# Kernel tuning notes

Hardware: AMD Instinct MI355X
Metric: run time of the kernel (lower is better)

The kernel has to match this reference:

```python
import jax, jax.numpy as jnp
import numpy as np

K = 4096          # infeatures
N = 12288         # outfeatures
M = 4096          # tokens (batch*seq)
GROUPSIZE = 128
G = K // GROUPSIZE  # 32 groups
PACK = 8          # 8 int4 nibbles per int32


def _unpack_int4(q):
    """Unpack int32 [R, C] -> int32 [R, C*8]; nibble j of word c maps to column c*8+j."""
    shifts = jnp.arange(0, 32, 4, dtype=jnp.int32)          # [8]
    nib = (q[:, :, None] >> shifts[None, None, :]) & 0xF    # [R, C, 8]
    return nib.reshape(q.shape[0], -1)


def setup_inputs() -> dict:
    key = jax.random.key(0)
    k1, k2, k3, k4, k5 = jax.random.split(key, 5)
    x = jax.random.normal(k1, (M, K), dtype=jnp.float32)
    qweight = jax.random.randint(k2, (K, N // PACK), 0, 2147483647, dtype=jnp.int32)
    qzeros = jax.random.randint(k3, (G, N // PACK), 0, 2147483647, dtype=jnp.int32)
    scales = jax.random.uniform(k4, (G, N), dtype=jnp.float32, minval=0.001, maxval=0.01)
    bias = jax.random.normal(k5, (N,), dtype=jnp.float32)
    return {"x": x, "qweight": qweight, "qzeros": qzeros, "scales": scales,
            "bias": bias, "groupsize": GROUPSIZE}


def reference(x, qweight, qzeros, scales, bias, groupsize):
    # Dequantize: w[k, n] = (q4[k, n] - z4[k//gs, n]) * scales[k//gs, n]
    w_int = _unpack_int4(qweight)                 # [K, N] int32, values 0..15
    z_int = _unpack_int4(qzeros)                  # [G, N] int32 (+1 already folded in)
    z_full = jnp.repeat(z_int, groupsize, axis=0)      # [K, N]
    s_full = jnp.repeat(scales, groupsize, axis=0)     # [K, N]
    weight = (w_int - z_full).astype(x.dtype) * s_full  # [K, N]
    out = x @ weight + bias                        # [M, N]
    return out
```

## Files before the change

### kernel.cpp

```cpp
#include <hip/hip_runtime.h>

#define M_DIM 4096
#define N_DIM 12288
#define K_DIM 4096
#define NP    1536
#define GS    128

typedef unsigned short ushort_t;
typedef _Float16 half8 __attribute__((ext_vector_type(8)));
typedef unsigned short us8 __attribute__((ext_vector_type(8)));
typedef float f32x16 __attribute__((ext_vector_type(16)));
typedef float f32x4 __attribute__((ext_vector_type(4)));

__device__ __forceinline__ unsigned short f2h(float f) {
  _Float16 h = (_Float16)f;
  return __builtin_bit_cast(unsigned short, h);
}

#define GLDS16(G, L) __builtin_amdgcn_global_load_lds(                      \
    (const __attribute__((address_space(1))) void*)(G),                     \
    (__attribute__((address_space(3))) void*)(L), 16, 0, 0)

#define DQ_BLOCKS (96 * 64)
#define CVT_BLOCKS (M_DIM * K_DIM / 16 / 256)

__global__ __launch_bounds__(256) void prep_kernel(
    const int* __restrict__ qw, const int* __restrict__ qz,
    const float* __restrict__ sc, ushort_t* __restrict__ wt,
    const float* __restrict__ x, ushort_t* __restrict__ xb) {
  __shared__ int ldsQ[64 * 16];
  __shared__ int ldsZ[16];
  const int tid = threadIdx.x;
  if (blockIdx.x >= DQ_BLOCKS) {
    size_t cid = (size_t)(blockIdx.x - DQ_BLOCKS) * 256 + tid;
    const float4* p = (const float4*)(x + cid * 16);
    float4 a = p[0], b = p[1], c = p[2], d = p[3];
    us8 o0, o1;
    o0[0] = f2h(a.x); o0[1] = f2h(a.y); o0[2] = f2h(a.z); o0[3] = f2h(a.w);
    o0[4] = f2h(b.x); o0[5] = f2h(b.y); o0[6] = f2h(b.z); o0[7] = f2h(b.w);
    o1[0] = f2h(c.x); o1[1] = f2h(c.y); o1[2] = f2h(c.z); o1[3] = f2h(c.w);
    o1[4] = f2h(d.x); o1[5] = f2h(d.y); o1[6] = f2h(d.z); o1[7] = f2h(d.w);
    *(us8*)(xb + cid * 16)     = o0;
    *(us8*)(xb + cid * 16 + 8) = o1;
    return;
  }
  const int bx = blockIdx.x % 96;
  const int by = blockIdx.x / 96;
  const int k0 = by * 64;
  const int n0 = bx * 128;
  const int w0 = n0 >> 3;
  const int g  = k0 >> 7;
  {
    int row = tid >> 2, qc = tid & 3;
    int4 v = *(const int4*)(qw + (size_t)(k0 + row) * NP + w0 + qc * 4);
    ldsQ[row * 16 + ((qc * 4 + 0) ^ (row & 15))] = v.x;
    ldsQ[row * 16 + ((qc * 4 + 1) ^ (row & 15))] = v.y;
    ldsQ[row * 16 + ((qc * 4 + 2) ^ (row & 15))] = v.z;
    ldsQ[row * 16 + ((qc * 4 + 3) ^ (row & 15))] = v.w;
  }
  if (tid < 16) ldsZ[tid] = qz[g * NP + w0 + tid];
  __syncthreads();
  const int nl  = tid >> 1;
  const int kh  = tid & 1;
  const int col = nl >> 3;
  const int j4  = (nl & 7) * 4;
  const int z   = (ldsZ[col] >> j4) & 0xF;
  const float s = sc[(size_t)g * N_DIM + n0 + nl];
  ushort_t* dst = wt + (size_t)(n0 + nl) * K_DIM + k0 + kh * 32;
#pragma unroll
  for (int c = 0; c < 4; ++c) {
    us8 o;
#pragma unroll
    for (int ii = 0; ii < 8; ++ii) {
      int row = kh * 32 + c * 8 + ii;
      int q = (ldsQ[row * 16 + (col ^ (row & 15))] >> j4) & 0xF;
      o[ii] = f2h((float)(q - z) * s);
    }
    *(us8*)(dst + c * 8) = o;
  }
}


__device__ __forceinline__ void stage_unit(
    int u, const ushort_t* __restrict__ Ag, const ushort_t* __restrict__ Bg,
    int m0, int n0, int tid, ushort_t* lds) {
  const int t   = u >> 1;
  const int ks  = u & 1;
  const int b   = t & 1;
  const int kbu = t * 64 + ks * 32;
  const int r   = tid >> 1;
  const int hp  = (tid & 1) ^ ((tid >> 3) & 1);
  const size_t ka = (size_t)kbu + hp * 8;
  ushort_t* dA = lds + b * 32768 + (2 * ks) * 4096 + tid * 8;
  ushort_t* dB = dA + 16384;
  const ushort_t* sA = Ag + (size_t)(m0 + r) * K_DIM + ka;
  const ushort_t* sB = Bg + (size_t)(n0 + r) * K_DIM + ka;
  GLDS16(sA,      dA);
  GLDS16(sA + 16, dA + 4096);
  GLDS16(sB,      dB);
  GLDS16(sB + 16, dB + 4096);
}

template <int N>
__device__ __forceinline__ void wait_lgkm() {
  if constexpr (N == 0)      asm volatile("s_waitcnt lgkmcnt(0)" ::: "memory");
  else if constexpr (N == 1) asm volatile("s_waitcnt lgkmcnt(1)" ::: "memory");
  else if constexpr (N == 2) asm volatile("s_waitcnt lgkmcnt(2)" ::: "memory");
  else if constexpr (N == 3) asm volatile("s_waitcnt lgkmcnt(3)" ::: "memory");
  else if constexpr (N == 4) asm volatile("s_waitcnt lgkmcnt(4)" ::: "memory");
  else if constexpr (N == 5) asm volatile("s_waitcnt lgkmcnt(5)" ::: "memory");
  else if constexpr (N == 6) asm volatile("s_waitcnt lgkmcnt(6)" ::: "memory");
  else if constexpr (N == 7) asm volatile("s_waitcnt lgkmcnt(7)" ::: "memory");
  __builtin_amdgcn_sched_barrier(0);
}

#define SB() __builtin_amdgcn_sched_barrier(0)

template <int VN, bool STG>
__device__ __forceinline__ void gemm_phase(
    int p, const ushort_t* __restrict__ Ag, const ushort_t* __restrict__ Bg,
    int m0, int n0, int tid, ushort_t* lds, f32x4 (&acc)[8][4]) {
  const int lane = tid & 63;
  const int wid  = tid >> 6;
  const int wm   = wid & 1;
  const int wn   = wid >> 1;
  const int ks   = p & 1;
  const int b    = (p >> 1) & 1;
  const int c  = lane >> 4;
  const int rl = lane & 15;
  const int sg = (c & 1) ^ ((rl >> 2) & 1);
  const ushort_t* base = lds + b * 32768 + (2 * ks + (c >> 1)) * 4096 + sg * 8;
  const ushort_t* pa = base + (wm * 128 + rl) * 16;
  const ushort_t* pb = base + 16384 + (wn * 64 + rl) * 16;
  half8 af[8], bf[4];
  af[0] = *(const half8*)(pa);
  bf[0] = *(const half8*)(pb);
  bf[1] = *(const half8*)(pb + 256);
  bf[2] = *(const half8*)(pb + 512);
  bf[3] = *(const half8*)(pb + 768);
  SB();
  af[1] = *(const half8*)(pa + 256);  SB();
  af[2] = *(const half8*)(pa + 512);  SB();
  af[3] = *(const half8*)(pa + 768);  SB();
  af[4] = *(const half8*)(pa + 1024); SB();
  af[5] = *(const half8*)(pa + 1280); SB();
  af[6] = *(const half8*)(pa + 1536); SB();
  af[7] = *(const half8*)(pa + 1792); SB();
  if constexpr (STG) stage_unit(p + 3, Ag, Bg, m0, n0, tid, lds);
  __builtin_amdgcn_s_setprio(1);
#define MFMA_ROW(i, W)                                                       \
  wait_lgkm<W>();                                                            \
  acc[i][0] = __builtin_amdgcn_mfma_f32_16x16x32_f16(af[i], bf[0], acc[i][0], 0, 0, 0); \
  acc[i][1] = __builtin_amdgcn_mfma_f32_16x16x32_f16(af[i], bf[1], acc[i][1], 0, 0, 0); \
  acc[i][2] = __builtin_amdgcn_mfma_f32_16x16x32_f16(af[i], bf[2], acc[i][2], 0, 0, 0); \
  acc[i][3] = __builtin_amdgcn_mfma_f32_16x16x32_f16(af[i], bf[3], acc[i][3], 0, 0, 0)
  MFMA_ROW(0, 7);
  MFMA_ROW(1, 6);
  MFMA_ROW(2, 5);
  MFMA_ROW(3, 4);
  MFMA_ROW(4, 3);
  MFMA_ROW(5, 2);
  MFMA_ROW(6, 1);
  MFMA_ROW(7, 0);
#undef MFMA_ROW
  __builtin_amdgcn_s_setprio(0);
  if constexpr (VN == 8)      asm volatile("s_waitcnt vmcnt(8)" ::: "memory");
  else if constexpr (VN == 4) asm volatile("s_waitcnt vmcnt(4)" ::: "memory");
  else if constexpr (VN == 0) asm volatile("s_waitcnt vmcnt(0)" ::: "memory");
  if constexpr (VN >= 0) {
    __builtin_amdgcn_s_barrier();
    asm volatile("" ::: "memory");
  }
}

__global__ __launch_bounds__(512, 2) void gemm256_kernel(
    const ushort_t* __restrict__ Xb, const ushort_t* __restrict__ Wt,
    const float* __restrict__ bias, float* __restrict__ out) {
  __shared__ __align__(16) ushort_t lds[65536];
  const int tid = threadIdx.x;
  const int m0  = blockIdx.x * 256;
  const int n0  = blockIdx.y * 256;
  f32x4 acc[8][4] = {};

  stage_unit(0, Xb, Wt, m0, n0, tid, lds);
  stage_unit(1, Xb, Wt, m0, n0, tid, lds);
  stage_unit(2, Xb, Wt, m0, n0, tid, lds);
  asm volatile("s_waitcnt vmcnt(8)" ::: "memory");
  __builtin_amdgcn_s_barrier();
  asm volatile("" ::: "memory");

#pragma unroll 4
  for (int p = 0; p < 125; ++p)
    gemm_phase<8, true>(p, Xb, Wt, m0, n0, tid, lds, acc);
  gemm_phase<4,  false>(125, Xb, Wt, m0, n0, tid, lds, acc);
  gemm_phase<0,  false>(126, Xb, Wt, m0, n0, tid, lds, acc);
  gemm_phase<-1, false>(127, Xb, Wt, m0, n0, tid, lds, acc);

  const int lane = tid & 63;
  const int wm   = (tid >> 6) & 1;
  const int wn   = tid >> 7;
#pragma unroll
  for (int jj = 0; jj < 4; ++jj) {
    int n = n0 + wn * 64 + jj * 16 + (lane & 15);
    float bv = bias[n];
#pragma unroll
    for (int i = 0; i < 8; ++i) {
      int mb = (int)(m0 + wm * 128 + i * 16 + ((lane >> 4) << 2));
#pragma unroll
      for (int r = 0; r < 4; ++r)
        __builtin_nontemporal_store(acc[i][jj][r] + bv,
                                    out + (size_t)(mb + r) * N_DIM + n);
    }
  }
}

template <int APRE, int BPRE>
__global__ __launch_bounds__(256) void gemm_kernel(
    const ushort_t* __restrict__ Xb, const float* __restrict__ Xf,
    const ushort_t* __restrict__ Wt,
    const int* __restrict__ qw, const int* __restrict__ qz,
    const float* __restrict__ sc,
    const float* __restrict__ bias, float* __restrict__ out) {
  __shared__ __align__(16) ushort_t lsA[128 * 64];
  __shared__ __align__(16) ushort_t lsB[128 * 64];
  const int tid  = threadIdx.x;
  const int lane = tid & 63;
  const int wid  = tid >> 6;
  const int wm   = wid & 1;
  const int wn   = wid >> 1;
  const int m0   = blockIdx.x * 128;
  const int n0   = blockIdx.y * 128;

  f32x16 acc[2][2] = {};

  for (int kt = 0; kt < K_DIM / 64; ++kt) {
    const int kb = kt * 64;
    if constexpr (APRE) {
#pragma unroll
      for (int i = 0; i < 4; ++i) {
        int cid = i * 256 + tid;
        int r = cid >> 3, scol = cid & 7;
        int c = scol ^ (r & 7);
        GLDS16(Xb + (size_t)(m0 + r) * K_DIM + kb + c * 8, lsA + cid * 8);
      }
    } else {
#pragma unroll
      for (int i = 0; i < 4; ++i) {
        int cid = i * 256 + tid;
        int r = cid >> 3, scol = cid & 7;
        int c = scol ^ (r & 7);
        const float* src = Xf + (size_t)(m0 + r) * K_DIM + kb + c * 8;
        float4 a = *(const float4*)src;
        float4 b = *(const float4*)(src + 4);
        us8 o;
        o[0] = f2h(a.x); o[1] = f2h(a.y); o[2] = f2h(a.z); o[3] = f2h(a.w);
        o[4] = f2h(b.x); o[5] = f2h(b.y); o[6] = f2h(b.z); o[7] = f2h(b.w);
        *(us8*)(lsA + cid * 8) = o;
      }
    }
    if constexpr (BPRE) {
#pragma unroll
      for (int i = 0; i < 4; ++i) {
        int cid = i * 256 + tid;
        int r = cid >> 3, scol = cid & 7;
        int c = scol ^ (r & 7);
        GLDS16(Wt + (size_t)(n0 + r) * K_DIM + kb + c * 8, lsB + cid * 8);
      }
    } else {
#pragma unroll
      for (int i = 0; i < 4; ++i) {
        int wi = i * 256 + tid;
        int kl = wi >> 4, cw = wi & 15;
        int k = kb + kl;
        int g = k >> 7;
        int qword = qw[(size_t)k * NP + (n0 >> 3) + cw];
        int zword = qz[g * NP + (n0 >> 3) + cw];
        float4 s0 = *(const float4*)(sc + (size_t)g * N_DIM + n0 + cw * 8);
        float4 s1 = *(const float4*)(sc + (size_t)g * N_DIM + n0 + cw * 8 + 4);
        float sv[8] = {s0.x, s0.y, s0.z, s0.w, s1.x, s1.y, s1.z, s1.w};
#pragma unroll
        for (int j = 0; j < 8; ++j) {
          int nl = cw * 8 + j;
          int q = (qword >> (4 * j)) & 0xF;
          int z = (zword >> (4 * j)) & 0xF;
          lsB[nl * 64 + (((kl >> 3) ^ (nl & 7)) << 3) + (kl & 7)] =
              f2h((float)(q - z) * sv[j]);
        }
      }
    }
    __syncthreads();
#pragma unroll
    for (int ks = 0; ks < 4; ++ks) {
      half8 af[2], bfr[2];
      const int h = lane >> 5;
      const int c = ks * 2 + h;
#pragma unroll
      for (int i = 0; i < 2; ++i) {
        int row = wm * 64 + i * 32 + (lane & 31);
        af[i] = *(const half8*)(lsA + (row * 8 + (c ^ (row & 7))) * 8);
      }
#pragma unroll
      for (int jj = 0; jj < 2; ++jj) {
        int row = wn * 64 + jj * 32 + (lane & 31);
        bfr[jj] = *(const half8*)(lsB + (row * 8 + (c ^ (row & 7))) * 8);
      }
#pragma unroll
      for (int i = 0; i < 2; ++i)
#pragma unroll
        for (int jj = 0; jj < 2; ++jj)
          acc[i][jj] = __builtin_amdgcn_mfma_f32_32x32x16_f16(
              af[i], bfr[jj], acc[i][jj], 0, 0, 0);
    }
    __syncthreads();
  }

#pragma unroll
  for (int jj = 0; jj < 2; ++jj) {
    int n = n0 + wn * 64 + jj * 32 + (lane & 31);
    float bv = bias[n];
#pragma unroll
    for (int i = 0; i < 2; ++i) {
      int mbase = m0 + wm * 64 + i * 32 + ((lane >> 5) << 2);
#pragma unroll
      for (int reg = 0; reg < 16; ++reg) {
        int m = mbase + (reg & 3) + ((reg >> 2) << 3);
        __builtin_nontemporal_store(acc[i][jj][reg] + bv,
                                    out + (size_t)m * N_DIM + n);
      }
    }
  }
}

extern "C" void kernel_launch(void* const* d_in, const int* in_sizes, int n_in,
                              void* d_out, int out_size, void* d_ws, size_t ws_size,
                              hipStream_t stream) {
  const float* x    = (const float*)d_in[0];
  const int*   qw   = (const int*)d_in[1];
  const int*   qz   = (const int*)d_in[2];
  const float* sc   = (const float*)d_in[3];
  const float* bias = (const float*)d_in[4];
  float*       out  = (float*)d_out;

  const size_t WT_BYTES = (size_t)N_DIM * K_DIM * 2;
  const size_t XB_BYTES = (size_t)M_DIM * K_DIM * 2;
  ushort_t* Wt = (ushort_t*)d_ws;
  ushort_t* Xb = (ushort_t*)((char*)d_ws + WT_BYTES);
  const bool hasWt = ws_size >= WT_BYTES;
  const bool hasXb = ws_size >= WT_BYTES + XB_BYTES;

  if (hasXb) {
    prep_kernel<<<DQ_BLOCKS + CVT_BLOCKS, 256, 0, stream>>>(qw, qz, sc, Wt, x, Xb);
    dim3 grid256(M_DIM / 256, N_DIM / 256);
    gemm256_kernel<<<grid256, 512, 0, stream>>>(Xb, Wt, bias, out);
  } else if (hasWt) {
    dim3 grid(M_DIM / 128, N_DIM / 128);
    prep_kernel<<<DQ_BLOCKS, 256, 0, stream>>>(qw, qz, sc, Wt, x, nullptr);
    gemm_kernel<0, 1><<<grid, 256, 0, stream>>>(nullptr, x, Wt, qw, qz, sc, bias, out);
  } else {
    dim3 grid(M_DIM / 128, N_DIM / 128);
    gemm_kernel<0, 0><<<grid, 256, 0, stream>>>(nullptr, x, nullptr, qw, qz, sc, bias, out);
  }
}
```

Measured before the change: 638.9 us.

## Pre-tile fp16 operands into LDS-ready swizzled blocks for contiguous staging

The prep kernel now writes dequantized weights and fp16 activations in a tiled layout. Each 256-row by 32-k slab is stored contiguously with the LDS swizzle baked in. The GEMM staging loads therefore become fully contiguous 16-byte global-to-LDS copies instead of strided row reads. The intent is better global load coalescing and simpler address math in the main loop, in exchange for a more complex prep-side shuffle. The unused intermediate fallback path is also removed.

```diff
diff --git a/kernel.cpp b/kernel.cpp
--- a/kernel.cpp
+++ b/kernel.cpp
@@ -9,6 +9,7 @@
 typedef unsigned short ushort_t;
 typedef _Float16 half8 __attribute__((ext_vector_type(8)));
 typedef unsigned short us8 __attribute__((ext_vector_type(8)));
+typedef unsigned short us16 __attribute__((ext_vector_type(16)));
 typedef float f32x16 __attribute__((ext_vector_type(16)));
 typedef float f32x4 __attribute__((ext_vector_type(4)));
 
@@ -21,84 +22,100 @@
     (const __attribute__((address_space(1))) void*)(G),                     \
     (__attribute__((address_space(3))) void*)(L), 16, 0, 0)
 
-#define DQ_BLOCKS (96 * 64)
-#define CVT_BLOCKS (M_DIM * K_DIM / 16 / 256)
+
+#define DQ_BLOCKS (48 * 128)
+#define CVT_BLOCKS (16 * 128)
 
 __global__ __launch_bounds__(256) void prep_kernel(
     const int* __restrict__ qw, const int* __restrict__ qz,
-    const float* __restrict__ sc, ushort_t* __restrict__ wt,
-    const float* __restrict__ x, ushort_t* __restrict__ xb) {
-  __shared__ int ldsQ[64 * 16];
-  __shared__ int ldsZ[16];
+    const float* __restrict__ sc, ushort_t* __restrict__ wtT,
+    const float* __restrict__ x, ushort_t* __restrict__ xbT) {
+  __shared__ int ldsQ[32 * 32];
+  __shared__ int ldsZ[32];
   const int tid = threadIdx.x;
-  if (blockIdx.x >= DQ_BLOCKS) {
-    size_t cid = (size_t)(blockIdx.x - DQ_BLOCKS) * 256 + tid;
-    const float4* p = (const float4*)(x + cid * 16);
-    float4 a = p[0], b = p[1], c = p[2], d = p[3];
-    us8 o0, o1;
-    o0[0] = f2h(a.x); o0[1] = f2h(a.y); o0[2] = f2h(a.z); o0[3] = f2h(a.w);
-    o0[4] = f2h(b.x); o0[5] = f2h(b.y); o0[6] = f2h(b.z); o0[7] = f2h(b.w);
-    o1[0] = f2h(c.x); o1[1] = f2h(c.y); o1[2] = f2h(c.z); o1[3] = f2h(c.w);
-    o1[4] = f2h(d.x); o1[5] = f2h(d.y); o1[6] = f2h(d.z); o1[7] = f2h(d.w);
-    *(us8*)(xb + cid * 16)     = o0;
-    *(us8*)(xb + cid * 16 + 8) = o1;
+  const int bx  = blockIdx.x;
+  if (bx >= DQ_BLOCKS) {
+    const int idx = bx - DQ_BLOCKS;
+    const int pm = idx >> 7, u = idx & 127;
+    const int r  = tid;
+    const int rb = (r >> 2) & 1;
+    const float* src = x + (size_t)(pm * 256 + r) * K_DIM + u * 32;
+    ushort_t* dst = xbT + (size_t)(pm * 128 + u) * 8192 + r * 16;
+#pragma unroll
+    for (int sl = 0; sl < 2; ++sl) {
+      float4 f0 = *(const float4*)(src + sl * 16);
+      float4 f1 = *(const float4*)(src + sl * 16 + 4);
+      float4 f2 = *(const float4*)(src + sl * 16 + 8);
+      float4 f3 = *(const float4*)(src + sl * 16 + 12);
+      us8 lo, hi;
+      lo[0] = f2h(f0.x); lo[1] = f2h(f0.y); lo[2] = f2h(f0.z); lo[3] = f2h(f0.w);
+      lo[4] = f2h(f1.x); lo[5] = f2h(f1.y); lo[6] = f2h(f1.z); lo[7] = f2h(f1.w);
+      hi[0] = f2h(f2.x); hi[1] = f2h(f2.y); hi[2] = f2h(f2.z); hi[3] = f2h(f2.w);
+      hi[4] = f2h(f3.x); hi[5] = f2h(f3.y); hi[6] = f2h(f3.z); hi[7] = f2h(f3.w);
+      us8 s0 = rb ? hi : lo;
+      us8 s1 = rb ? lo : hi;
+      us16 o = __builtin_shufflevector(s0, s1, 0, 1, 2, 3, 4, 5, 6, 7,
+                                       8, 9, 10, 11, 12, 13, 14, 15);
+      *(us16*)(dst + sl * 4096) = o;
+    }
     return;
   }
-  const int bx = blockIdx.x % 96;
-  const int by = blockIdx.x / 96;
-  const int k0 = by * 64;
-  const int n0 = bx * 128;
-  const int w0 = n0 >> 3;
-  const int g  = k0 >> 7;
+  const int p  = bx >> 7;
+  const int u  = bx & 127;
+  const int w0 = p << 5;
+  const int g  = u >> 2;
+  const int kb = u << 5;
   {
-    int row = tid >> 2, qc = tid & 3;
-    int4 v = *(const int4*)(qw + (size_t)(k0 + row) * NP + w0 + qc * 4);
-    ldsQ[row * 16 + ((qc * 4 + 0) ^ (row & 15))] = v.x;
-    ldsQ[row * 16 + ((qc * 4 + 1) ^ (row & 15))] = v.y;
-    ldsQ[row * 16 + ((qc * 4 + 2) ^ (row & 15))] = v.z;
-    ldsQ[row * 16 + ((qc * 4 + 3) ^ (row & 15))] = v.w;
-  }
-  if (tid < 16) ldsZ[tid] = qz[g * NP + w0 + tid];
+    int row = tid >> 3, wq = tid & 7;
+    int4 v = *(const int4*)(qw + (size_t)(kb + row) * NP + w0 + wq * 4);
+    ldsQ[row * 32 + ((wq * 4 + 0) ^ row)] = v.x;
+    ldsQ[row * 32 + ((wq * 4 + 1) ^ row)] = v.y;
+    ldsQ[row * 32 + ((wq * 4 + 2) ^ row)] = v.z;
+    ldsQ[row * 32 + ((wq * 4 + 3) ^ row)] = v.w;
+  }
+  if (tid < 32) ldsZ[tid] = qz[(size_t)g * NP + w0 + tid];
   __syncthreads();
-  const int nl  = tid >> 1;
-  const int kh  = tid & 1;
-  const int col = nl >> 3;
-  const int j4  = (nl & 7) * 4;
+  const int r   = tid;
+  const int col = r >> 3;
+  const int j4  = (r & 7) * 4;
+  const int rb  = (r >> 2) & 1;
   const int z   = (ldsZ[col] >> j4) & 0xF;
-  const float s = sc[(size_t)g * N_DIM + n0 + nl];
-  ushort_t* dst = wt + (size_t)(n0 + nl) * K_DIM + k0 + kh * 32;
-#pragma unroll
-  for (int c = 0; c < 4; ++c) {
-    us8 o;
-#pragma unroll
-    for (int ii = 0; ii < 8; ++ii) {
-      int row = kh * 32 + c * 8 + ii;
-      int q = (ldsQ[row * 16 + (col ^ (row & 15))] >> j4) & 0xF;
-      o[ii] = f2h((float)(q - z) * s);
-    }
-    *(us8*)(dst + c * 8) = o;
+  const float s = sc[(size_t)g * N_DIM + p * 256 + r];
+  ushort_t* dst = wtT + (size_t)(p * 128 + u) * 8192 + r * 16;
+#pragma unroll
+  for (int sl = 0; sl < 2; ++sl) {
+    us8 e0, e1;
+#pragma unroll
+    for (int j = 0; j < 8; ++j) {
+      int k0 = sl * 16 + j;
+      int k1 = k0 + 8;
+      int q0 = (ldsQ[k0 * 32 + (col ^ k0)] >> j4) & 0xF;
+      int q1 = (ldsQ[k1 * 32 + (col ^ k1)] >> j4) & 0xF;
+      e0[j] = f2h((float)(q0 - z) * s);
+      e1[j] = f2h((float)(q1 - z) * s);
+    }
+    us8 s0 = rb ? e1 : e0;
+    us8 s1 = rb ? e0 : e1;
+    us16 o = __builtin_shufflevector(s0, s1, 0, 1, 2, 3, 4, 5, 6, 7,
+                                     8, 9, 10, 11, 12, 13, 14, 15);
+    *(us16*)(dst + sl * 4096) = o;
   }
 }
 
 
 __device__ __forceinline__ void stage_unit(
-    int u, const ushort_t* __restrict__ Ag, const ushort_t* __restrict__ Bg,
-    int m0, int n0, int tid, ushort_t* lds) {
-  const int t   = u >> 1;
-  const int ks  = u & 1;
-  const int b   = t & 1;
-  const int kbu = t * 64 + ks * 32;
-  const int r   = tid >> 1;
-  const int hp  = (tid & 1) ^ ((tid >> 3) & 1);
-  const size_t ka = (size_t)kbu + hp * 8;
-  ushort_t* dA = lds + b * 32768 + (2 * ks) * 4096 + tid * 8;
+    int u, const ushort_t* __restrict__ AT, const ushort_t* __restrict__ BT,
+    int pm, int pn, int tid, ushort_t* lds) {
+  const int b  = (u >> 1) & 1;
+  const int ks = u & 1;
+  ushort_t* dA = lds + b * 32768 + ks * 8192 + tid * 8;
   ushort_t* dB = dA + 16384;
-  const ushort_t* sA = Ag + (size_t)(m0 + r) * K_DIM + ka;
-  const ushort_t* sB = Bg + (size_t)(n0 + r) * K_DIM + ka;
-  GLDS16(sA,      dA);
-  GLDS16(sA + 16, dA + 4096);
-  GLDS16(sB,      dB);
-  GLDS16(sB + 16, dB + 4096);
+  const ushort_t* sA = AT + (size_t)(pm * 128 + u) * 8192 + tid * 8;
+  const ushort_t* sB = BT + (size_t)(pn * 128 + u) * 8192 + tid * 8;
+  GLDS16(sA,        dA);
+  GLDS16(sA + 4096, dA + 4096);
+  GLDS16(sB,        dB);
+  GLDS16(sB + 4096, dB + 4096);
 }
 
 template <int N>
@@ -118,8 +135,8 @@
 
 template <int VN, bool STG>
 __device__ __forceinline__ void gemm_phase(
-    int p, const ushort_t* __restrict__ Ag, const ushort_t* __restrict__ Bg,
-    int m0, int n0, int tid, ushort_t* lds, f32x4 (&acc)[8][4]) {
+    int p, const ushort_t* __restrict__ AT, const ushort_t* __restrict__ BT,
+    int pm, int pn, int tid, ushort_t* lds, f32x4 (&acc)[8][4]) {
   const int lane = tid & 63;
   const int wid  = tid >> 6;
   const int wm   = wid & 1;
@@ -146,7 +163,7 @@
   af[5] = *(const half8*)(pa + 1280); SB();
   af[6] = *(const half8*)(pa + 1536); SB();
   af[7] = *(const half8*)(pa + 1792); SB();
-  if constexpr (STG) stage_unit(p + 3, Ag, Bg, m0, n0, tid, lds);
+  if constexpr (STG) stage_unit(p + 3, AT, BT, pm, pn, tid, lds);
   __builtin_amdgcn_s_setprio(1);
 #define MFMA_ROW(i, W)                                                       \
   wait_lgkm<W>();                                                            \
@@ -174,27 +191,29 @@
 }
 
 __global__ __launch_bounds__(512, 2) void gemm256_kernel(
-    const ushort_t* __restrict__ Xb, const ushort_t* __restrict__ Wt,
+    const ushort_t* __restrict__ XbT, const ushort_t* __restrict__ WtT,
     const float* __restrict__ bias, float* __restrict__ out) {
   __shared__ __align__(16) ushort_t lds[65536];
   const int tid = threadIdx.x;
-  const int m0  = blockIdx.x * 256;
-  const int n0  = blockIdx.y * 256;
+  const int pm  = blockIdx.x;
+  const int pn  = blockIdx.y;
+  const int m0  = pm * 256;
+  const int n0  = pn * 256;
   f32x4 acc[8][4] = {};
 
-  stage_unit(0, Xb, Wt, m0, n0, tid, lds);
-  stage_unit(1, Xb, Wt, m0, n0, tid, lds);
-  stage_unit(2, Xb, Wt, m0, n0, tid, lds);
+  stage_unit(0, XbT, WtT, pm, pn, tid, lds);
+  stage_unit(1, XbT, WtT, pm, pn, tid, lds);
+  stage_unit(2, XbT, WtT, pm, pn, tid, lds);
   asm volatile("s_waitcnt vmcnt(8)" ::: "memory");
   __builtin_amdgcn_s_barrier();
   asm volatile("" ::: "memory");
 
 #pragma unroll 4
   for (int p = 0; p < 125; ++p)
-    gemm_phase<8, true>(p, Xb, Wt, m0, n0, tid, lds, acc);
-  gemm_phase<4,  false>(125, Xb, Wt, m0, n0, tid, lds, acc);
-  gemm_phase<0,  false>(126, Xb, Wt, m0, n0, tid, lds, acc);
-  gemm_phase<-1, false>(127, Xb, Wt, m0, n0, tid, lds, acc);
+    gemm_phase<8, true>(p, XbT, WtT, pm, pn, tid, lds, acc);
+  gemm_phase<4,  false>(125, XbT, WtT, pm, pn, tid, lds, acc);
+  gemm_phase<0,  false>(126, XbT, WtT, pm, pn, tid, lds, acc);
+  gemm_phase<-1, false>(127, XbT, WtT, pm, pn, tid, lds, acc);
 
   const int lane = tid & 63;
   const int wm   = (tid >> 6) & 1;
@@ -214,10 +233,8 @@
   }
 }
 
-template <int APRE, int BPRE>
-__global__ __launch_bounds__(256) void gemm_kernel(
-    const ushort_t* __restrict__ Xb, const float* __restrict__ Xf,
-    const ushort_t* __restrict__ Wt,
+__global__ __launch_bounds__(256) void gemm_fused_kernel(
+    const float* __restrict__ Xf,
     const int* __restrict__ qw, const int* __restrict__ qz,
     const float* __restrict__ sc,
     const float* __restrict__ bias, float* __restrict__ out) {
@@ -235,57 +252,37 @@
 
   for (int kt = 0; kt < K_DIM / 64; ++kt) {
     const int kb = kt * 64;
-    if constexpr (APRE) {
-#pragma unroll
-      for (int i = 0; i < 4; ++i) {
-        int cid = i * 256 + tid;
-        int r = cid >> 3, scol = cid & 7;
-        int c = scol ^ (r & 7);
-        GLDS16(Xb + (size_t)(m0 + r) * K_DIM + kb + c * 8, lsA + cid * 8);
-      }
-    } else {
-#pragma unroll
-      for (int i = 0; i < 4; ++i) {
-        int cid = i * 256 + tid;
-        int r = cid >> 3, scol = cid & 7;
-        int c = scol ^ (r & 7);
-        const float* src = Xf + (size_t)(m0 + r) * K_DIM + kb + c * 8;
-        float4 a = *(const float4*)src;
-        float4 b = *(const float4*)(src + 4);
-        us8 o;
-        o[0] = f2h(a.x); o[1] = f2h(a.y); o[2] = f2h(a.z); o[3] = f2h(a.w);
-        o[4] = f2h(b.x); o[5] = f2h(b.y); o[6] = f2h(b.z); o[7] = f2h(b.w);
-        *(us8*)(lsA + cid * 8) = o;
-      }
-    }
-    if constexpr (BPRE) {
-#pragma unroll
-      for (int i = 0; i < 4; ++i) {
-        int cid = i * 256 + tid;
-        int r = cid >> 3, scol = cid & 7;
-        int c = scol ^ (r & 7);
-        GLDS16(Wt + (size_t)(n0 + r) * K_DIM + kb + c * 8, lsB + cid * 8);
-      }
-    } else {
-#pragma unroll
-      for (int i = 0; i < 4; ++i) {
-        int wi = i * 256 + tid;
-        int kl = wi >> 4, cw = wi & 15;
-        int k = kb + kl;
-        int g = k >> 7;
-        int qword = qw[(size_t)k * NP + (n0 >> 3) + cw];
-        int zword = qz[g * NP + (n0 >> 3) + cw];
-        float4 s0 = *(const float4*)(sc + (size_t)g * N_DIM + n0 + cw * 8);
-        float4 s1 = *(const float4*)(sc + (size_t)g * N_DIM + n0 + cw * 8 + 4);
-        float sv[8] = {s0.x, s0.y, s0.z, s0.w, s1.x, s1.y, s1.z, s1.w};
-#pragma unroll
-        for (int j = 0; j < 8; ++j) {
-          int nl = cw * 8 + j;
-          int q = (qword >> (4 * j)) & 0xF;
-          int z = (zword >> (4 * j)) & 0xF;
-          lsB[nl * 64 + (((kl >> 3) ^ (nl & 7)) << 3) + (kl & 7)] =
-              f2h((float)(q - z) * sv[j]);
-        }
+#pragma unroll
+    for (int i = 0; i < 4; ++i) {
+      int cid = i * 256 + tid;
+      int r = cid >> 3, scol = cid & 7;
+      int c = scol ^ (r & 7);
+      const float* src = Xf + (size_t)(m0 + r) * K_DIM + kb + c * 8;
+      float4 a = *(const float4*)src;
+      float4 b = *(const float4*)(src + 4);
+      us8 o;
+      o[0] = f2h(a.x); o[1] = f2h(a.y); o[2] = f2h(a.z); o[3] = f2h(a.w);
+      o[4] = f2h(b.x); o[5] = f2h(b.y); o[6] = f2h(b.z); o[7] = f2h(b.w);
+      *(us8*)(lsA + cid * 8) = o;
+    }
+#pragma unroll
+    for (int i = 0; i < 4; ++i) {
+      int wi = i * 256 + tid;
+      int kl = wi >> 4, cw = wi & 15;
+      int k = kb + kl;
+      int g = k >> 7;
+      int qword = qw[(size_t)k * NP + (n0 >> 3) + cw];
+      int zword = qz[g * NP + (n0 >> 3) + cw];
+      float4 s0 = *(const float4*)(sc + (size_t)g * N_DIM + n0 + cw * 8);
+      float4 s1 = *(const float4*)(sc + (size_t)g * N_DIM + n0 + cw * 8 + 4);
+      float sv[8] = {s0.x, s0.y, s0.z, s0.w, s1.x, s1.y, s1.z, s1.w};
+#pragma unroll
+      for (int j = 0; j < 8; ++j) {
+        int nl = cw * 8 + j;
+        int q = (qword >> (4 * j)) & 0xF;
+        int z = (zword >> (4 * j)) & 0xF;
+        lsB[nl * 64 + (((kl >> 3) ^ (nl & 7)) << 3) + (kl & 7)] =
+            f2h((float)(q - z) * sv[j]);
       }
     }
     __syncthreads();
@@ -343,21 +340,16 @@
 
   const size_t WT_BYTES = (size_t)N_DIM * K_DIM * 2;
   const size_t XB_BYTES = (size_t)M_DIM * K_DIM * 2;
-  ushort_t* Wt = (ushort_t*)d_ws;
-  ushort_t* Xb = (ushort_t*)((char*)d_ws + WT_BYTES);
-  const bool hasWt = ws_size >= WT_BYTES;
-  const bool hasXb = ws_size >= WT_BYTES + XB_BYTES;
-
-  if (hasXb) {
-    prep_kernel<<<DQ_BLOCKS + CVT_BLOCKS, 256, 0, stream>>>(qw, qz, sc, Wt, x, Xb);
+  ushort_t* WtT = (ushort_t*)d_ws;
+  ushort_t* XbT = (ushort_t*)((char*)d_ws + WT_BYTES);
+  const bool hasWs = ws_size >= WT_BYTES + XB_BYTES;
+
+  if (hasWs) {
+    prep_kernel<<<DQ_BLOCKS + CVT_BLOCKS, 256, 0, stream>>>(qw, qz, sc, WtT, x, XbT);
     dim3 grid256(M_DIM / 256, N_DIM / 256);
-    gemm256_kernel<<<grid256, 512, 0, stream>>>(Xb, Wt, bias, out);
-  } else if (hasWt) {
-    dim3 grid(M_DIM / 128, N_DIM / 128);
-    prep_kernel<<<DQ_BLOCKS, 256, 0, stream>>>(qw, qz, sc, Wt, x, nullptr);
-    gemm_kernel<0, 1><<<grid, 256, 0, stream>>>(nullptr, x, Wt, qw, qz, sc, bias, out);
+    gemm256_kernel<<<grid256, 512, 0, stream>>>(XbT, WtT, bias, out);
   } else {
     dim3 grid(M_DIM / 128, N_DIM / 128);
-    gemm_kernel<0, 0><<<grid, 256, 0, stream>>>(nullptr, x, nullptr, qw, qz, sc, bias, out);
-  }
-}
+    gemm_fused_kernel<<<grid, 256, 0, stream>>>(x, qw, qz, sc, bias, out);
+  }
+}
```

Result: faster. 591.1 us (-7.5%).
